# Kernel tuning notes

Hardware: AMD Instinct MI355X
Metric: run time of the kernel (lower is better)

The kernel has to match this reference:

```python
import jax, jax.numpy as jnp
import numpy as np

N = 8192          # num_nodes (feature dim == node count, x is square)
H = N // 2        # hidden channels of conv1
NUM_GRAPHS = 8    # graphs in the batch for global_mean_pool
EDGE_P = 0.004    # adjacency density -> avg degree ~33


def setup_inputs() -> dict:
    key = jax.random.key(0)
    kx, kb, k1, k2 = jax.random.split(key, 4)
    # sparse binary adjacency-as-features: nonzero(x) defines the edge list
    x = (jax.random.uniform(kx, (N, N)) < EDGE_P).astype(jnp.float32)
    batch = jnp.sort(jax.random.randint(kb, (N,), 0, NUM_GRAPHS))
    # GCNConv weights (lin has no bias in PyG; separate additive bias)
    W1 = jax.random.normal(k1, (N, H), jnp.float32) / np.sqrt(N)
    b1 = jnp.zeros((H,), jnp.float32)
    W2 = jax.random.normal(k2, (H, N), jnp.float32) / np.sqrt(H)
    b2 = jnp.zeros((N,), jnp.float32)
    return {"x": x, "W1": W1, "b1": b1, "W2": W2, "b2": b2, "batch": batch}


def _gcn_norm_adj(x):
    """Symmetric-normalized adjacency implied by edge_index = nonzero(x).

    PyG GCNConv: edges (r -> c) for every nonzero x[r, c], unit edge weight,
    remaining self loops added, deg = in-degree of target, message to node c is
    deg^-1/2[r] * deg^-1/2[c] * xw[r]. Since x is square/dense we express the
    aggregation as a dense normalized-adjacency matmul (identical math).
    """
    A = (x != 0).astype(x.dtype)                # [N, N], A[r, c] = edge r->c
    idx = jnp.arange(A.shape[0])
    A = A.at[idx, idx].set(1.0)                 # add (remaining) self loops
    deg = A.sum(axis=0)                         # in-degree of each target node
    dinv = jax.lax.rsqrt(deg)                   # deg >= 1 (self loops)
    return dinv[:, None] * A * dinv[None, :]    # B[r, c] = dinv[r]*A[r,c]*dinv[c]


def reference(x, W1, b1, W2, b2, batch):
    B = _gcn_norm_adj(x)
    # conv1: aggregate_c sum_r B[r, c] * (x @ W1)[r]  == B.T @ (x @ W1)
    h = jax.nn.relu(B.T @ (x @ W1) + b1)        # [N, H]
    h = B.T @ (h @ W2) + b2                     # [N, N]
    # global_mean_pool over graph assignment `batch`
    sums = jax.ops.segment_sum(h, batch, num_segments=NUM_GRAPHS)
    cnt = jax.ops.segment_sum(jnp.ones((h.shape[0],), h.dtype), batch,
                              num_segments=NUM_GRAPHS)
    return sums / jnp.maximum(cnt, 1.0)[:, None]  # [NUM_GRAPHS, N]
```

## Files before the change

kernel.cpp:

```cpp
#include <hip/hip_runtime.h>
#include <hip/hip_bf16.h>

#define NN 8192
#define HH 4096
#define GG 8
#define STR 128
#define NCH 32
#define PRG 64
#define FJG 32

typedef unsigned uint4n __attribute__((ext_vector_type(4)));

__device__ inline unsigned bf16rne(float f) {
    unsigned u = __float_as_uint(f);
    unsigned r = 0x7fffu + ((u >> 16) & 1u);
    return (u + r) >> 16;
}
__device__ inline unsigned pack2(float lo, float hi) {
    return bf16rne(lo) | (bf16rne(hi) << 16);
}
__device__ inline void nt_store16(void* p, unsigned a, unsigned b, unsigned c, unsigned d) {
    uint4n v; v.x = a; v.y = b; v.z = c; v.w = d;
    __builtin_nontemporal_store(v, reinterpret_cast<uint4n*>(p));
}
__device__ inline void acc2p(float2& acc, unsigned u) {
    float2 t;
    t.x = __uint_as_float(u << 16);
    t.y = __uint_as_float(u & 0xffff0000u);
    asm("v_pk_add_f32 %0, %1, %0" : "+v"(acc) : "v"(t));
}
__device__ inline void unpack8(uint4 v, float* __restrict__ h) {
    const unsigned* pu = reinterpret_cast<const unsigned*>(&v);
    #pragma unroll
    for (int q = 0; q < 4; ++q) {
        const unsigned u = pu[q];
        h[2 * q]     = __uint_as_float(u << 16);
        h[2 * q + 1] = __uint_as_float(u & 0xffff0000u);
    }
}

__global__ __launch_bounds__(256) void k_cvt(const float* __restrict__ src,
                                             uint4* __restrict__ dst) {
    const size_t i = (size_t)blockIdx.x * 256 + threadIdx.x;
    const float4 a = reinterpret_cast<const float4*>(src)[2 * i];
    const float4 b = reinterpret_cast<const float4*>(src)[2 * i + 1];
    nt_store16(&dst[i], pack2(a.x, a.y), pack2(a.z, a.w),
                        pack2(b.x, b.y), pack2(b.z, b.w));
}

__global__ __launch_bounds__(256) void k_build(const float* __restrict__ x,
                                               unsigned* __restrict__ colfill,
                                               unsigned* __restrict__ degX,
                                               unsigned* __restrict__ degA,
                                               unsigned* __restrict__ csrX,
                                               unsigned* __restrict__ csrA,
                                               unsigned* __restrict__ cscA) {
    const int r = blockIdx.x;
    __shared__ unsigned px, pa;
    if (threadIdx.x == 0) { px = 0u; pa = 0u; }
    __syncthreads();
    const float4* xr = reinterpret_cast<const float4*>(x + (size_t)r * NN);
    #pragma unroll
    for (int i = 0; i < NN / (4 * 256); ++i) {
        const int c4 = i * 256 + threadIdx.x;
        float4 v = xr[c4];
        const float* vp = reinterpret_cast<const float*>(&v);
        #pragma unroll
        for (int k = 0; k < 4; ++k) {
            const int c = c4 * 4 + k;
            const bool nzx = (vp[k] != 0.0f);
            const bool nzA = nzx || (c == r);
            if (nzx) {
                unsigned p = atomicAdd(&px, 1u);
                if (p < STR) csrX[(size_t)r * STR + p] = (unsigned)c << 13;
            }
            if (nzA) {
                unsigned p = atomicAdd(&pa, 1u);
                if (p < STR) csrA[(size_t)r * STR + p] = (unsigned)c;
                unsigned q = atomicAdd(&colfill[c], 1u);
                if (q < STR) cscA[(size_t)c * STR + q] = (unsigned)r << 13;
            }
        }
    }
    __syncthreads();
    if (threadIdx.x == 0) { degX[r] = px; degA[r] = pa; }
}

__global__ __launch_bounds__(256) void k_prep(const unsigned* __restrict__ colfill,
                                              const int* __restrict__ batch,
                                              float* __restrict__ dinv,
                                              unsigned* __restrict__ cnt) {
    const int i = blockIdx.x * 256 + threadIdx.x;
    dinv[i] = rsqrtf((float)colfill[i]);
    atomicAdd(&cnt[batch[i]], 1u);
}

__global__ __launch_bounds__(256) void k_s(const unsigned* __restrict__ degA,
                                           const unsigned* __restrict__ csrA,
                                           const float* __restrict__ dinv,
                                           const int* __restrict__ batch,
                                           float* __restrict__ s) {
    const int r = blockIdx.x * 256 + threadIdx.x;
    unsigned deg = degA[r];
    if (deg > STR) deg = STR;
    float bins[GG];
    #pragma unroll
    for (int g = 0; g < GG; ++g) bins[g] = 0.0f;
    for (unsigned e = 0; e < deg; ++e) {
        const unsigned c = csrA[(size_t)r * STR + e];
        const float d = dinv[c];
        const int gb = batch[c];
        #pragma unroll
        for (int g = 0; g < GG; ++g) bins[g] += (gb == g) ? d : 0.0f;
    }
    const float dr = dinv[r];
    #pragma unroll
    for (int g = 0; g < GG; ++g) s[(size_t)g * NN + r] = dr * bins[g];
}

__global__ __launch_bounds__(256) void k_spmm1(const char* __restrict__ W1b,
                                               const unsigned* __restrict__ degX,
                                               const unsigned* __restrict__ csrX,
                                               const float* __restrict__ dinv,
                                               unsigned* __restrict__ Mh) {
    const unsigned L = blockIdx.x;
    const int xcd   = L & 7;
    const unsigned k = L >> 3;
    const int phase = k >> 11;
    const int pix   = k & 2047;
    const int ch    = xcd + (phase << 3);
    int node = (pix << 2) | (threadIdx.x >> 6);
    node = __builtin_amdgcn_readfirstlane(node);
    const int lane = threadIdx.x & 63;

    unsigned deg = degX[node];
    if (deg > STR) deg = STR;
    const unsigned* __restrict__ el = csrX + (size_t)node * STR;
    const unsigned loff = (unsigned)(ch * 64 + lane) * 4u;

    float2 acc = make_float2(0.f, 0.f);
    unsigned e = 0;
    for (; e + 8 <= deg; e += 8) {
        unsigned o0 = el[e + 0], o1 = el[e + 1], o2 = el[e + 2], o3 = el[e + 3];
        unsigned o4 = el[e + 4], o5 = el[e + 5], o6 = el[e + 6], o7 = el[e + 7];
        const unsigned v0 = *reinterpret_cast<const unsigned*>(W1b + (o0 + loff));
        const unsigned v1 = *reinterpret_cast<const unsigned*>(W1b + (o1 + loff));
        const unsigned v2 = *reinterpret_cast<const unsigned*>(W1b + (o2 + loff));
        const unsigned v3 = *reinterpret_cast<const unsigned*>(W1b + (o3 + loff));
        const unsigned v4 = *reinterpret_cast<const unsigned*>(W1b + (o4 + loff));
        const unsigned v5 = *reinterpret_cast<const unsigned*>(W1b + (o5 + loff));
        const unsigned v6 = *reinterpret_cast<const unsigned*>(W1b + (o6 + loff));
        const unsigned v7 = *reinterpret_cast<const unsigned*>(W1b + (o7 + loff));
        acc2p(acc, v0); acc2p(acc, v1); acc2p(acc, v2); acc2p(acc, v3);
        acc2p(acc, v4); acc2p(acc, v5); acc2p(acc, v6); acc2p(acc, v7);
    }
    for (; e < deg; ++e) {
        unsigned o = el[e];
        acc2p(acc, *reinterpret_cast<const unsigned*>(W1b + (o + loff)));
    }

    const float dr = dinv[node];
    __builtin_nontemporal_store(pack2(dr * acc.x, dr * acc.y),
                                &Mh[(size_t)node * (HH / 2) + ch * 64 + lane]);
}

__global__ __launch_bounds__(256) void k_conv1(const char* __restrict__ Mb,
                                               const float* __restrict__ b1,
                                               const float* __restrict__ dinv,
                                               const unsigned* __restrict__ colfill,
                                               const unsigned* __restrict__ cscA,
                                               unsigned* __restrict__ hB) {
    const unsigned L = blockIdx.x;
    const int xcd   = L & 7;
    const unsigned k = L >> 3;
    const int phase = k >> 11;
    const int pix   = k & 2047;
    const int ch    = xcd + (phase << 3);
    int node = (pix << 2) | (threadIdx.x >> 6);
    node = __builtin_amdgcn_readfirstlane(node);
    const int lane = threadIdx.x & 63;

    unsigned deg = colfill[node];
    if (deg > STR) deg = STR;
    const unsigned* __restrict__ el = cscA + (size_t)node * STR;
    const unsigned loff = (unsigned)(ch * 64 + lane) * 4u;

    float2 acc = make_float2(0.f, 0.f);
    unsigned e = 0;
    for (; e + 8 <= deg; e += 8) {
        unsigned o0 = el[e + 0], o1 = el[e + 1], o2 = el[e + 2], o3 = el[e + 3];
        unsigned o4 = el[e + 4], o5 = el[e + 5], o6 = el[e + 6], o7 = el[e + 7];
        const unsigned v0 = *reinterpret_cast<const unsigned*>(Mb + (o0 + loff));
        const unsigned v1 = *reinterpret_cast<const unsigned*>(Mb + (o1 + loff));
        const unsigned v2 = *reinterpret_cast<const unsigned*>(Mb + (o2 + loff));
        const unsigned v3 = *reinterpret_cast<const unsigned*>(Mb + (o3 + loff));
        const unsigned v4 = *reinterpret_cast<const unsigned*>(Mb + (o4 + loff));
        const unsigned v5 = *reinterpret_cast<const unsigned*>(Mb + (o5 + loff));
        const unsigned v6 = *reinterpret_cast<const unsigned*>(Mb + (o6 + loff));
        const unsigned v7 = *reinterpret_cast<const unsigned*>(Mb + (o7 + loff));
        acc2p(acc, v0); acc2p(acc, v1); acc2p(acc, v2); acc2p(acc, v3);
        acc2p(acc, v4); acc2p(acc, v5); acc2p(acc, v6); acc2p(acc, v7);
    }
    for (; e < deg; ++e) {
        unsigned o = el[e];
        acc2p(acc, *reinterpret_cast<const unsigned*>(Mb + (o + loff)));
    }

    const float dc = dinv[node];
    const float2 bv = reinterpret_cast<const float2*>(b1)[ch * 64 + lane];
    const float h0 = fmaxf(fmaf(dc, acc.x, bv.x), 0.0f);
    const float h1 = fmaxf(fmaf(dc, acc.y, bv.y), 0.0f);
    __builtin_nontemporal_store(pack2(h0, h1),
                                &hB[(size_t)node * (HH / 2) + ch * 64 + lane]);
}

__global__ __launch_bounds__(256) void k_poolA(const uint4* __restrict__ hB,
                                               const float* __restrict__ s,
                                               float* __restrict__ part) {
    const int j = blockIdx.x * 256 + threadIdx.x;
    const int c0 = blockIdx.y * (NN / PRG);
    __shared__ float s_t[GG * (NN / PRG)];
    for (int i = threadIdx.x; i < GG * (NN / PRG); i += 256) {
        const int g = i / (NN / PRG);
        const int cc = i % (NN / PRG);
        s_t[i] = s[(size_t)g * NN + c0 + cc];
    }
    __syncthreads();
    float tacc[GG][8];
    #pragma unroll
    for (int g = 0; g < GG; ++g)
        #pragma unroll
        for (int q = 0; q < 8; ++q) tacc[g][q] = 0.0f;
    for (int cc = 0; cc < NN / PRG; ++cc) {
        const uint4 v = hB[(size_t)(c0 + cc) * (HH / 8) + j];
        float hv[8];
        unpack8(v, hv);
        #pragma unroll
        for (int g = 0; g < GG; ++g) {
            const float sv = s_t[g * (NN / PRG) + cc];
            #pragma unroll
            for (int q = 0; q < 8; ++q) tacc[g][q] = fmaf(sv, hv[q], tacc[g][q]);
        }
    }
    float4* p4 = reinterpret_cast<float4*>(part);
    #pragma unroll
    for (int g = 0; g < GG; ++g) {
        const size_t base = ((size_t)(blockIdx.y * GG + g) * HH) / 4 + j * 2;
        p4[base]     = make_float4(tacc[g][0], tacc[g][1], tacc[g][2], tacc[g][3]);
        p4[base + 1] = make_float4(tacc[g][4], tacc[g][5], tacc[g][6], tacc[g][7]);
    }
}

__global__ __launch_bounds__(256) void k_poolB(const float* __restrict__ part,
                                               float* __restrict__ t) {
    const int idx = blockIdx.x * 256 + threadIdx.x;
    const int g = idx / (HH / 4);
    const int j4 = idx % (HH / 4);
    const float4* p4 = reinterpret_cast<const float4*>(part);
    float4 acc = make_float4(0.f, 0.f, 0.f, 0.f);
    for (int rg = 0; rg < PRG; ++rg) {
        const float4 v = p4[((size_t)(rg * GG + g) * HH) / 4 + j4];
        acc.x += v.x; acc.y += v.y; acc.z += v.z; acc.w += v.w;
    }
    reinterpret_cast<float4*>(t)[idx] = acc;
}

__global__ __launch_bounds__(256) void k_final(const float* __restrict__ W2,
                                               const float* __restrict__ t,
                                               const unsigned* __restrict__ cnt,
                                               float* __restrict__ part2) {
    __shared__ float tld[GG * 128];
    const int tj = threadIdx.x;
    const int j0 = blockIdx.y * 128;
    const int nbase = blockIdx.x * 1024;
    for (int i = threadIdx.x; i < GG * 128; i += 256) {
        const int g = i >> 7;
        const int jj = i & 127;
        unsigned c = cnt[g];
        if (c < 1u) c = 1u;
        tld[i] = t[(size_t)g * HH + j0 + jj] * (1.0f / (float)c);
    }
    __syncthreads();
    float4 acc[GG];
    #pragma unroll
    for (int g = 0; g < GG; ++g) acc[g] = make_float4(0.f, 0.f, 0.f, 0.f);
    for (int jj = 0; jj < 128; ++jj) {
        const int jv = j0 + jj;
        float4 w = reinterpret_cast<const float4*>(W2 + (size_t)jv * NN + nbase)[tj];
        #pragma unroll
        for (int g = 0; g < GG; ++g) {
            const float tv = tld[g * 128 + jj];
            acc[g].x = fmaf(tv, w.x, acc[g].x);
            acc[g].y = fmaf(tv, w.y, acc[g].y);
            acc[g].z = fmaf(tv, w.z, acc[g].z);
            acc[g].w = fmaf(tv, w.w, acc[g].w);
        }
    }
    float4* p4 = reinterpret_cast<float4*>(part2);
    #pragma unroll
    for (int g = 0; g < GG; ++g)
        p4[((size_t)(blockIdx.y * GG + g) * NN + nbase) / 4 + tj] = acc[g];
}

__global__ __launch_bounds__(256) void k_fin2(const float* __restrict__ part2,
                                              const float* __restrict__ b2,
                                              float* __restrict__ out) {
    const int idx = blockIdx.x * 256 + threadIdx.x;
    const int g = idx / (NN / 4);
    const int n4 = idx % (NN / 4);
    const float4* p4 = reinterpret_cast<const float4*>(part2);
    float4 acc = reinterpret_cast<const float4*>(b2)[n4];
    for (int jg = 0; jg < FJG; ++jg) {
        const float4 v = p4[((size_t)(jg * GG + g) * NN) / 4 + n4];
        acc.x += v.x; acc.y += v.y; acc.z += v.z; acc.w += v.w;
    }
    reinterpret_cast<float4*>(out)[idx] = acc;
}

extern "C" void kernel_launch(void* const* d_in, const int* in_sizes, int n_in,
                              void* d_out, int out_size, void* d_ws, size_t ws_size,
                              hipStream_t stream) {
    const float* x  = (const float*)d_in[0];
    const float* W1 = (const float*)d_in[1];
    const float* b1 = (const float*)d_in[2];
    const float* W2 = (const float*)d_in[3];
    const float* b2 = (const float*)d_in[4];
    const int* batch = (const int*)d_in[5];
    float* out = (float*)d_out;

    char* ws = (char*)d_ws;
    size_t off = 0;
    auto alloc = [&](size_t bytes) -> char* {
        char* p = ws + off;
        off = (off + bytes + 255) & ~(size_t)255;
        return p;
    };
    uint4*    Mh      = (uint4*)   alloc((size_t)NN * HH * 2);
    uint4*    W1h     = (uint4*)   alloc((size_t)NN * HH * 2);
    uint4*    hB      = W1h;
    char*     zbegin  = ws + off;
    float*    t       = (float*)   alloc((size_t)GG * HH * 4);
    unsigned* colfill = (unsigned*)alloc((size_t)NN * 4);
    unsigned* cnt     = (unsigned*)alloc((size_t)GG * 4);
    char*     zend    = ws + off;
    float*    s       = (float*)   alloc((size_t)GG * NN * 4);
    float*    dinv    = (float*)   alloc((size_t)NN * 4);
    unsigned* degX    = (unsigned*)alloc((size_t)NN * 4);
    unsigned* degA    = (unsigned*)alloc((size_t)NN * 4);
    unsigned* csrX    = (unsigned*)alloc((size_t)NN * STR * 4);
    unsigned* csrA    = (unsigned*)alloc((size_t)NN * STR * 4);
    unsigned* cscA    = (unsigned*)alloc((size_t)NN * STR * 4);
    float*    part    = (float*)csrX;
    float*    part2   = (float*)csrX;
    (void)ws_size; (void)in_sizes; (void)n_in; (void)out_size;

    hipMemsetAsync(zbegin, 0, (size_t)(zend - zbegin), stream);

    k_cvt<<<(NN * HH / 8) / 256, 256, 0, stream>>>(W1, (uint4*)W1h);
    k_build<<<NN, 256, 0, stream>>>(x, colfill, degX, degA, csrX, csrA, cscA);
    k_prep<<<NN / 256, 256, 0, stream>>>(colfill, batch, dinv, cnt);
    k_s<<<NN / 256, 256, 0, stream>>>(degA, csrA, dinv, batch, s);
    k_spmm1<<<(NN / 4) * NCH, 256, 0, stream>>>((const char*)W1h, degX, csrX, dinv,
                                                (unsigned*)Mh);
    k_conv1<<<(NN / 4) * NCH, 256, 0, stream>>>((const char*)Mh, b1, dinv, colfill, cscA,
                                                (unsigned*)hB);
    k_poolA<<<dim3(HH / 2048, PRG), 256, 0, stream>>>(hB, s, part);
    k_poolB<<<(GG * HH / 4) / 256, 256, 0, stream>>>(part, t);
    k_final<<<dim3(NN / 1024, FJG), 256, 0, stream>>>(W2, t, cnt, part2);
    k_fin2<<<(GG * NN / 4) / 256, 256, 0, stream>>>(part2, b2, out);
}
```

Baseline: 640.1 us.

## Fuse dinv prep into consumers and loop four channels per SpMM block

Removes the k_prep kernel and the dinv buffer: rsqrt of colfill is recomputed inline in k_s, k_spmm1 and k_conv1, and the per-graph node count is folded into k_s. The two SpMM kernels now launch 4x fewer blocks, each looping over 4 channel chunks and reusing the same node's edge list and degree. This cuts one launch and the repeated index and degree loads per block. In exchange there is less parallelism per launch and longer serial work per wave.

Measured after the change: 693.8 us. 8.4% more time.

```diff
diff --git a/kernel.cpp b/kernel.cpp
--- a/kernel.cpp
+++ b/kernel.cpp
@@ -86,21 +86,14 @@
     if (threadIdx.x == 0) { degX[r] = px; degA[r] = pa; }
 }
 
-__global__ __launch_bounds__(256) void k_prep(const unsigned* __restrict__ colfill,
-                                              const int* __restrict__ batch,
-                                              float* __restrict__ dinv,
-                                              unsigned* __restrict__ cnt) {
-    const int i = blockIdx.x * 256 + threadIdx.x;
-    dinv[i] = rsqrtf((float)colfill[i]);
-    atomicAdd(&cnt[batch[i]], 1u);
-}
-
 __global__ __launch_bounds__(256) void k_s(const unsigned* __restrict__ degA,
                                            const unsigned* __restrict__ csrA,
-                                           const float* __restrict__ dinv,
+                                           const unsigned* __restrict__ colfill,
                                            const int* __restrict__ batch,
-                                           float* __restrict__ s) {
+                                           float* __restrict__ s,
+                                           unsigned* __restrict__ cnt) {
     const int r = blockIdx.x * 256 + threadIdx.x;
+    atomicAdd(&cnt[batch[r]], 1u);
     unsigned deg = degA[r];
     if (deg > STR) deg = STR;
     float bins[GG];
@@ -108,12 +101,12 @@
     for (int g = 0; g < GG; ++g) bins[g] = 0.0f;
     for (unsigned e = 0; e < deg; ++e) {
         const unsigned c = csrA[(size_t)r * STR + e];
-        const float d = dinv[c];
+        const float d = rsqrtf((float)colfill[c]);
         const int gb = batch[c];
         #pragma unroll
         for (int g = 0; g < GG; ++g) bins[g] += (gb == g) ? d : 0.0f;
     }
-    const float dr = dinv[r];
+    const float dr = rsqrtf((float)colfill[r]);
     #pragma unroll
     for (int g = 0; g < GG; ++g) s[(size_t)g * NN + r] = dr * bins[g];
 }
@@ -121,14 +114,11 @@
 __global__ __launch_bounds__(256) void k_spmm1(const char* __restrict__ W1b,
                                                const unsigned* __restrict__ degX,
                                                const unsigned* __restrict__ csrX,
-                                               const float* __restrict__ dinv,
+                                               const unsigned* __restrict__ colfill,
                                                unsigned* __restrict__ Mh) {
     const unsigned L = blockIdx.x;
-    const int xcd   = L & 7;
-    const unsigned k = L >> 3;
-    const int phase = k >> 11;
-    const int pix   = k & 2047;
-    const int ch    = xcd + (phase << 3);
+    const int xcd = L & 7;
+    const int pix = L >> 3;
     int node = (pix << 2) | (threadIdx.x >> 6);
     node = __builtin_amdgcn_readfirstlane(node);
     const int lane = threadIdx.x & 63;
@@ -136,82 +126,84 @@
     unsigned deg = degX[node];
     if (deg > STR) deg = STR;
     const unsigned* __restrict__ el = csrX + (size_t)node * STR;
-    const unsigned loff = (unsigned)(ch * 64 + lane) * 4u;
-
-    float2 acc = make_float2(0.f, 0.f);
-    unsigned e = 0;
-    for (; e + 8 <= deg; e += 8) {
-        unsigned o0 = el[e + 0], o1 = el[e + 1], o2 = el[e + 2], o3 = el[e + 3];
-        unsigned o4 = el[e + 4], o5 = el[e + 5], o6 = el[e + 6], o7 = el[e + 7];
-        const unsigned v0 = *reinterpret_cast<const unsigned*>(W1b + (o0 + loff));
-        const unsigned v1 = *reinterpret_cast<const unsigned*>(W1b + (o1 + loff));
-        const unsigned v2 = *reinterpret_cast<const unsigned*>(W1b + (o2 + loff));
-        const unsigned v3 = *reinterpret_cast<const unsigned*>(W1b + (o3 + loff));
-        const unsigned v4 = *reinterpret_cast<const unsigned*>(W1b + (o4 + loff));
-        const unsigned v5 = *reinterpret_cast<const unsigned*>(W1b + (o5 + loff));
-        const unsigned v6 = *reinterpret_cast<const unsigned*>(W1b + (o6 + loff));
-        const unsigned v7 = *reinterpret_cast<const unsigned*>(W1b + (o7 + loff));
-        acc2p(acc, v0); acc2p(acc, v1); acc2p(acc, v2); acc2p(acc, v3);
-        acc2p(acc, v4); acc2p(acc, v5); acc2p(acc, v6); acc2p(acc, v7);
-    }
-    for (; e < deg; ++e) {
-        unsigned o = el[e];
-        acc2p(acc, *reinterpret_cast<const unsigned*>(W1b + (o + loff)));
-    }
-
-    const float dr = dinv[node];
-    __builtin_nontemporal_store(pack2(dr * acc.x, dr * acc.y),
-                                &Mh[(size_t)node * (HH / 2) + ch * 64 + lane]);
+    const float dr = rsqrtf((float)colfill[node]);
+
+    #pragma unroll
+    for (int p = 0; p < 4; ++p) {
+        const int ch = xcd + (p << 3);
+        const unsigned loff = (unsigned)(ch * 64 + lane) * 4u;
+        float2 acc = make_float2(0.f, 0.f);
+        unsigned e = 0;
+        for (; e + 8 <= deg; e += 8) {
+            unsigned o0 = el[e + 0], o1 = el[e + 1], o2 = el[e + 2], o3 = el[e + 3];
+            unsigned o4 = el[e + 4], o5 = el[e + 5], o6 = el[e + 6], o7 = el[e + 7];
+            const unsigned v0 = *reinterpret_cast<const unsigned*>(W1b + (o0 + loff));
+            const unsigned v1 = *reinterpret_cast<const unsigned*>(W1b + (o1 + loff));
+            const unsigned v2 = *reinterpret_cast<const unsigned*>(W1b + (o2 + loff));
+            const unsigned v3 = *reinterpret_cast<const unsigned*>(W1b + (o3 + loff));
+            const unsigned v4 = *reinterpret_cast<const unsigned*>(W1b + (o4 + loff));
+            const unsigned v5 = *reinterpret_cast<const unsigned*>(W1b + (o5 + loff));
+            const unsigned v6 = *reinterpret_cast<const unsigned*>(W1b + (o6 + loff));
+            const unsigned v7 = *reinterpret_cast<const unsigned*>(W1b + (o7 + loff));
+            acc2p(acc, v0); acc2p(acc, v1); acc2p(acc, v2); acc2p(acc, v3);
+            acc2p(acc, v4); acc2p(acc, v5); acc2p(acc, v6); acc2p(acc, v7);
+        }
+        for (; e < deg; ++e) {
+            unsigned o = el[e];
+            acc2p(acc, *reinterpret_cast<const unsigned*>(W1b + (o + loff)));
+        }
+        __builtin_nontemporal_store(pack2(dr * acc.x, dr * acc.y),
+                                    &Mh[(size_t)node * (HH / 2) + ch * 64 + lane]);
+    }
 }
 
 __global__ __launch_bounds__(256) void k_conv1(const char* __restrict__ Mb,
                                                const float* __restrict__ b1,
-                                               const float* __restrict__ dinv,
                                                const unsigned* __restrict__ colfill,
                                                const unsigned* __restrict__ cscA,
                                                unsigned* __restrict__ hB) {
     const unsigned L = blockIdx.x;
-    const int xcd   = L & 7;
-    const unsigned k = L >> 3;
-    const int phase = k >> 11;
-    const int pix   = k & 2047;
-    const int ch    = xcd + (phase << 3);
+    const int xcd = L & 7;
+    const int pix = L >> 3;
     int node = (pix << 2) | (threadIdx.x >> 6);
     node = __builtin_amdgcn_readfirstlane(node);
     const int lane = threadIdx.x & 63;
 
     unsigned deg = colfill[node];
+    const float dc = rsqrtf((float)deg);
     if (deg > STR) deg = STR;
     const unsigned* __restrict__ el = cscA + (size_t)node * STR;
-    const unsigned loff = (unsigned)(ch * 64 + lane) * 4u;
-
-    float2 acc = make_float2(0.f, 0.f);
-    unsigned e = 0;
-    for (; e + 8 <= deg; e += 8) {
-        unsigned o0 = el[e + 0], o1 = el[e + 1], o2 = el[e + 2], o3 = el[e + 3];
-        unsigned o4 = el[e + 4], o5 = el[e + 5], o6 = el[e + 6], o7 = el[e + 7];
-        const unsigned v0 = *reinterpret_cast<const unsigned*>(Mb + (o0 + loff));
-        const unsigned v1 = *reinterpret_cast<const unsigned*>(Mb + (o1 + loff));
-        const unsigned v2 = *reinterpret_cast<const unsigned*>(Mb + (o2 + loff));
-        const unsigned v3 = *reinterpret_cast<const unsigned*>(Mb + (o3 + loff));
-        const unsigned v4 = *reinterpret_cast<const unsigned*>(Mb + (o4 + loff));
-        const unsigned v5 = *reinterpret_cast<const unsigned*>(Mb + (o5 + loff));
-        const unsigned v6 = *reinterpret_cast<const unsigned*>(Mb + (o6 + loff));
-        const unsigned v7 = *reinterpret_cast<const unsigned*>(Mb + (o7 + loff));
-        acc2p(acc, v0); acc2p(acc, v1); acc2p(acc, v2); acc2p(acc, v3);
-        acc2p(acc, v4); acc2p(acc, v5); acc2p(acc, v6); acc2p(acc, v7);
-    }
-    for (; e < deg; ++e) {
-        unsigned o = el[e];
-        acc2p(acc, *reinterpret_cast<const unsigned*>(Mb + (o + loff)));
-    }
-
-    const float dc = dinv[node];
-    const float2 bv = reinterpret_cast<const float2*>(b1)[ch * 64 + lane];
-    const float h0 = fmaxf(fmaf(dc, acc.x, bv.x), 0.0f);
-    const float h1 = fmaxf(fmaf(dc, acc.y, bv.y), 0.0f);
-    __builtin_nontemporal_store(pack2(h0, h1),
-                                &hB[(size_t)node * (HH / 2) + ch * 64 + lane]);
+
+    #pragma unroll
+    for (int p = 0; p < 4; ++p) {
+        const int ch = xcd + (p << 3);
+        const unsigned loff = (unsigned)(ch * 64 + lane) * 4u;
+        float2 acc = make_float2(0.f, 0.f);
+        unsigned e = 0;
+        for (; e + 8 <= deg; e += 8) {
+            unsigned o0 = el[e + 0], o1 = el[e + 1], o2 = el[e + 2], o3 = el[e + 3];
+            unsigned o4 = el[e + 4], o5 = el[e + 5], o6 = el[e + 6], o7 = el[e + 7];
+            const unsigned v0 = *reinterpret_cast<const unsigned*>(Mb + (o0 + loff));
+            const unsigned v1 = *reinterpret_cast<const unsigned*>(Mb + (o1 + loff));
+            const unsigned v2 = *reinterpret_cast<const unsigned*>(Mb + (o2 + loff));
+            const unsigned v3 = *reinterpret_cast<const unsigned*>(Mb + (o3 + loff));
+            const unsigned v4 = *reinterpret_cast<const unsigned*>(Mb + (o4 + loff));
+            const unsigned v5 = *reinterpret_cast<const unsigned*>(Mb + (o5 + loff));
+            const unsigned v6 = *reinterpret_cast<const unsigned*>(Mb + (o6 + loff));
+            const unsigned v7 = *reinterpret_cast<const unsigned*>(Mb + (o7 + loff));
+            acc2p(acc, v0); acc2p(acc, v1); acc2p(acc, v2); acc2p(acc, v3);
+            acc2p(acc, v4); acc2p(acc, v5); acc2p(acc, v6); acc2p(acc, v7);
+        }
+        for (; e < deg; ++e) {
+            unsigned o = el[e];
+            acc2p(acc, *reinterpret_cast<const unsigned*>(Mb + (o + loff)));
+        }
+        const float2 bv = reinterpret_cast<const float2*>(b1)[ch * 64 + lane];
+        const float h0 = fmaxf(fmaf(dc, acc.x, bv.x), 0.0f);
+        const float h1 = fmaxf(fmaf(dc, acc.y, bv.y), 0.0f);
+        __builtin_nontemporal_store(pack2(h0, h1),
+                                    &hB[(size_t)node * (HH / 2) + ch * 64 + lane]);
+    }
 }
 
 __global__ __launch_bounds__(256) void k_poolA(const uint4* __restrict__ hB,
@@ -344,7 +336,6 @@
     unsigned* cnt     = (unsigned*)alloc((size_t)GG * 4);
     char*     zend    = ws + off;
     float*    s       = (float*)   alloc((size_t)GG * NN * 4);
-    float*    dinv    = (float*)   alloc((size_t)NN * 4);
     unsigned* degX    = (unsigned*)alloc((size_t)NN * 4);
     unsigned* degA    = (unsigned*)alloc((size_t)NN * 4);
     unsigned* csrX    = (unsigned*)alloc((size_t)NN * STR * 4);
@@ -358,12 +349,11 @@
 
     k_cvt<<<(NN * HH / 8) / 256, 256, 0, stream>>>(W1, (uint4*)W1h);
     k_build<<<NN, 256, 0, stream>>>(x, colfill, degX, degA, csrX, csrA, cscA);
-    k_prep<<<NN / 256, 256, 0, stream>>>(colfill, batch, dinv, cnt);
-    k_s<<<NN / 256, 256, 0, stream>>>(degA, csrA, dinv, batch, s);
-    k_spmm1<<<(NN / 4) * NCH, 256, 0, stream>>>((const char*)W1h, degX, csrX, dinv,
-                                                (unsigned*)Mh);
-    k_conv1<<<(NN / 4) * NCH, 256, 0, stream>>>((const char*)Mh, b1, dinv, colfill, cscA,
-                                                (unsigned*)hB);
+    k_s<<<NN / 256, 256, 0, stream>>>(degA, csrA, colfill, batch, s, cnt);
+    k_spmm1<<<(NN / 4) * 8, 256, 0, stream>>>((const char*)W1h, degX, csrX, colfill,
+                                              (unsigned*)Mh);
+    k_conv1<<<(NN / 4) * 8, 256, 0, stream>>>((const char*)Mh, b1, colfill, cscA,
+                                              (unsigned*)hB);
     k_poolA<<<dim3(HH / 2048, PRG), 256, 0, stream>>>(hB, s, part);
     k_poolB<<<(GG * HH / 4) / 256, 256, 0, stream>>>(part, t);
     k_final<<<dim3(NN / 1024, FJG), 256, 0, stream>>>(W2, t, cnt, part2);
```
